# Kernel optimization log

Hardware: AMD Instinct MI355X
Metric: run time of the kernel (lower is better)

Reference implementation:

```python
import jax, jax.numpy as jnp
import numpy as np

D, H, DH, L, FF, P, IMG, NPR = 768, 12, 64, 12, 3072, 16, 224, 8
SCALE = 0.125  # 1/sqrt(64), hardcoded in source
DEEP_G = 12


def layernorm(x, g, b, eps=1e-5):
    mu = jnp.mean(x, axis=-1, keepdims=True)
    var = jnp.var(x, axis=-1, keepdims=True)
    return (x - mu) * jax.lax.rsqrt(var + eps) * g + b


def quick_gelu(x):  # CLIP's QuickGELU
    return x * jax.nn.sigmoid(1.702 * x)


def setup_inputs() -> dict:
    key = jax.random.key(0)
    ks = jax.random.split(key, 32)
    rn = lambda k, shape, s=0.02: (jax.random.normal(k, shape, jnp.float32) * s)
    B = 64
    return {
        "image": jax.random.normal(ks[0], (B, 3, IMG, IMG), jnp.float32),
        "g_prompt": rn(ks[1], (B, L, NPR, D)),
        "patch_w": rn(ks[2], (D, 3, P, P)),            # OIHW conv kernel (no bias in CLIP)
        "cls_emb": rn(ks[3], (D,)),
        "pos_emb": rn(ks[4], (1 + (IMG // P) ** 2, D)),  # [197, 768]
        "pre_g": jnp.ones((D,)), "pre_b": jnp.zeros((D,)),
        "ln1_g": jnp.ones((L, D)), "ln1_b": jnp.zeros((L, D)),
        "qw": rn(ks[5], (L, D, D)), "qb": jnp.zeros((L, D)),
        "kw": rn(ks[6], (L, D, D)), "kb": jnp.zeros((L, D)),
        "vw": rn(ks[7], (L, D, D)), "vb": jnp.zeros((L, D)),
        "ow": rn(ks[8], (L, D, D)), "ob": jnp.zeros((L, D)),
        "ln2_g": jnp.ones((L, D)), "ln2_b": jnp.zeros((L, D)),
        "fc1_w": rn(ks[9], (L, FF, D)), "fc1_b": jnp.zeros((L, FF)),
        "fc2_w": rn(ks[10], (L, D, FF)), "fc2_b": jnp.zeros((L, D)),
        "post_g": jnp.ones((D,)), "post_b": jnp.zeros((D,)),
    }


def reference(image, g_prompt, patch_w, cls_emb, pos_emb, pre_g, pre_b,
              ln1_g, ln1_b, qw, qb, kw, kb, vw, vb, ow, ob,
              ln2_g, ln2_b, fc1_w, fc1_b, fc2_w, fc2_b, post_g, post_b):
    B = image.shape[0]
    # --- embeddings: patch conv (stride=patch, VALID), flatten, prepend CLS, add pos ---
    feat = jax.lax.conv_general_dilated(
        image, patch_w, window_strides=(P, P), padding="VALID",
        dimension_numbers=("NCHW", "OIHW", "NCHW"))          # [B, D, 14, 14]
    feat = feat.reshape(B, D, -1).transpose(0, 2, 1)           # [B, 196, D]
    cls = jnp.broadcast_to(cls_emb, (B, 1, D))
    x = jnp.concatenate([cls, feat], axis=1) + pos_emb[None]   # [B, 197, D]
    # --- append prompts for layer 0, pre-layernorm ---
    x = jnp.concatenate([x, g_prompt[:, 0]], axis=1)           # [B, 205, D]
    x = layernorm(x, pre_g, pre_b)
    S = x.shape[1]
    for i in range(L):
        if i > 0 and i < DEEP_G:  # replace method: swap in fresh prompts
            x = jnp.concatenate([x[:, :-NPR], g_prompt[:, i]], axis=1)
        # --- attention ---
        res = x
        h = layernorm(x, ln1_g[i], ln1_b[i])
        q = (jnp.einsum("bsd,od->bso", h, qw[i]) + qb[i]) * SCALE
        k = jnp.einsum("bsd,od->bso", h, kw[i]) + kb[i]
        v = jnp.einsum("bsd,od->bso", h, vw[i]) + vb[i]
        q = q.reshape(B, S, H, DH)
        k = k.reshape(B, S, H, DH)
        v = v.reshape(B, S, H, DH)
        w = jnp.einsum("bihd,bjhd->bhij", q, k)
        w = jax.nn.softmax(w, axis=-1)
        a = jnp.einsum("bhij,bjhd->bihd", w, v).reshape(B, S, D)
        x = res + (jnp.einsum("bsd,od->bso", a, ow[i]) + ob[i])
        # --- MLP (QuickGELU) ---
        res = x
        h = layernorm(x, ln2_g[i], ln2_b[i])
        h = quick_gelu(jnp.einsum("bsd,fd->bsf", h, fc1_w[i]) + fc1_b[i])
        x = res + (jnp.einsum("bsf,df->bsd", h, fc2_w[i]) + fc2_b[i])
    return layernorm(x[:, 0, :], post_g, post_b)               # [B, D]
```

## Files before the change

kernel.cpp:

```cpp
#include <hip/hip_runtime.h>
#include <hip/hip_bf16.h>

typedef __hip_bfloat16 bf16;
typedef __attribute__((ext_vector_type(8))) __bf16 bf16x8;
typedef __attribute__((ext_vector_type(4))) float f32x4;

static constexpr int B_   = 64;
static constexpr int S_   = 205;
static constexpr int D_   = 768;
static constexpr int FF_  = 3072;
static constexpr int L_   = 12;
static constexpr int MTOK = B_ * S_;
static constexpr int MPAD = 13184;
static constexpr int MP_  = 12544;

static constexpr size_t OFF_QKVW = 0;
static constexpr size_t OFF_OW   = OFF_QKVW + (size_t)12*2304*768*2;
static constexpr size_t OFF_FC1W = OFF_OW   + (size_t)12*768*768*2;
static constexpr size_t OFF_FC2W = OFF_FC1W + (size_t)12*3072*768*2;
static constexpr size_t OFF_PW   = OFF_FC2W + (size_t)12*768*3072*2;
static constexpr size_t OFF_QKVB = OFF_PW   + (size_t)768*768*2;
static constexpr size_t OFF_X    = OFF_QKVB + (size_t)12*2304*4;
static constexpr size_t OFF_H    = OFF_X    + (size_t)MPAD*768*4;
static constexpr size_t OFF_QKV  = OFF_H    + (size_t)MPAD*768*2;
static constexpr size_t OFF_FF   = OFF_QKV  + (size_t)MPAD*2304*2;

__device__ __forceinline__ f32x4 mfma16(bf16x8 a, bf16x8 b, f32x4 c) {
  return __builtin_amdgcn_mfma_f32_16x16x32_bf16(a, b, c, 0, 0, 0);
}

__device__ __forceinline__ void async_ld16(const bf16* g, bf16* l) {
  __builtin_amdgcn_global_load_lds(
      (const __attribute__((address_space(1))) unsigned int*)g,
      (__attribute__((address_space(3))) unsigned int*)l, 16, 0, 0);
}

__global__ __launch_bounds__(256) void cvt_bf16_kernel(const float* __restrict__ src,
                                                       bf16* __restrict__ dst, int n4) {
  int i = blockIdx.x * 256 + threadIdx.x;
  if (i >= n4) return;
  float4 v = ((const float4*)src)[i];
  int e = i * 4;
  dst[e + 0] = __float2bfloat16(v.x);
  dst[e + 1] = __float2bfloat16(v.y);
  dst[e + 2] = __float2bfloat16(v.z);
  dst[e + 3] = __float2bfloat16(v.w);
}

__global__ __launch_bounds__(256) void cvt_qkvw_kernel(const float* __restrict__ qw,
    const float* __restrict__ kw, const float* __restrict__ vw, bf16* __restrict__ dst) {
  int i = blockIdx.x * 256 + threadIdx.x;
  const int total = 12 * 2304 * 768 / 4;
  if (i >= total) return;
  int e = i * 4;
  int l = e / (2304 * 768);
  int r = e - l * (2304 * 768);
  int o = r / 768;
  int d = r - o * 768;
  const float* src;
  if (o < 768)       src = qw + ((size_t)l * 768 + o) * 768 + d;
  else if (o < 1536) src = kw + ((size_t)l * 768 + (o - 768)) * 768 + d;
  else               src = vw + ((size_t)l * 768 + (o - 1536)) * 768 + d;
  float4 v = *(const float4*)src;
  dst[e + 0] = __float2bfloat16(v.x);
  dst[e + 1] = __float2bfloat16(v.y);
  dst[e + 2] = __float2bfloat16(v.z);
  dst[e + 3] = __float2bfloat16(v.w);
}

__global__ __launch_bounds__(256) void cvt_qkvb_kernel(const float* __restrict__ qb,
    const float* __restrict__ kb, const float* __restrict__ vb, float* __restrict__ dst) {
  int i = blockIdx.x * 256 + threadIdx.x;
  if (i >= 12 * 2304) return;
  int l = i / 2304, o = i - l * 2304;
  float v = (o < 768) ? qb[l * 768 + o] : (o < 1536) ? kb[l * 768 + o - 768] : vb[l * 768 + o - 1536];
  dst[i] = v;
}

__global__ __launch_bounds__(256) void im2col_kernel(const float* __restrict__ img,
                                                     bf16* __restrict__ dst) {
  int idx = blockIdx.x * 256 + threadIdx.x;
  if (idx >= MP_ * 768) return;
  int k = idx % 768;
  int m = idx / 768;
  int b = m / 196, p = m - b * 196;
  int py = p / 14, px = p - py * 14;
  int c = k >> 8, rr = k & 255, kh = rr >> 4, kw_ = rr & 15;
  dst[idx] = __float2bfloat16(img[((size_t)(b * 3 + c) * 224 + py * 16 + kh) * 224 + px * 16 + kw_]);
}

__global__ __launch_bounds__(256) void assemble_kernel(const float* __restrict__ feat,
    const float* __restrict__ cls, const float* __restrict__ pos,
    const float* __restrict__ gp, float* __restrict__ x) {
  int idx = blockIdx.x * 256 + threadIdx.x;
  if (idx >= MTOK * 768) return;
  int d = idx % 768;
  int t = idx / 768;
  int s = t % 205;
  int b = t / 205;
  float v;
  if (s == 0)        v = cls[d] + pos[d];
  else if (s < 197)  v = feat[((size_t)b * 196 + (s - 1)) * 768 + d] + pos[(size_t)s * 768 + d];
  else               v = gp[(((size_t)b * 12 + 0) * 8 + (s - 197)) * 768 + d];
  x[idx] = v;
}

__global__ __launch_bounds__(256) void prompt_replace_kernel(const float* __restrict__ gp,
                                                             float* __restrict__ x, int layer) {
  int idx = blockIdx.x * 256 + threadIdx.x;
  if (idx >= B_ * 8 * 768) return;
  int d = idx % 768;
  int t = idx / 768;
  int j = t & 7, b = t >> 3;
  x[((size_t)(b * 205 + 197 + j)) * 768 + d] = gp[(((size_t)b * 12 + layer) * 8 + j) * 768 + d];
}

__global__ __launch_bounds__(256) void ln_kernel(const float* __restrict__ x, int irs,
    const float* __restrict__ g, const float* __restrict__ be,
    void* __restrict__ out, int ors, int out_bf16, int nrows) {
  int row = blockIdx.x * 4 + (threadIdx.x >> 6);
  if (row >= nrows) return;
  int lane = threadIdx.x & 63;
  const float* xr = x + (size_t)row * irs;
  float v[12];
  float s = 0.f;
#pragma unroll
  for (int i = 0; i < 12; ++i) { v[i] = xr[lane + 64 * i]; s += v[i]; }
#pragma unroll
  for (int m = 1; m < 64; m <<= 1) s += __shfl_xor(s, m, 64);
  float mu = s * (1.f / 768.f);
  float ss = 0.f;
#pragma unroll
  for (int i = 0; i < 12; ++i) { float dd = v[i] - mu; ss += dd * dd; }
#pragma unroll
  for (int m = 1; m < 64; m <<= 1) ss += __shfl_xor(ss, m, 64);
  float rstd = rsqrtf(ss * (1.f / 768.f) + 1e-5f);
#pragma unroll
  for (int i = 0; i < 12; ++i) {
    int d = lane + 64 * i;
    float o = (v[i] - mu) * rstd * g[d] + be[d];
    if (out_bf16) ((bf16*)out)[(size_t)row * ors + d] = __float2bfloat16(o);
    else          ((float*)out)[(size_t)row * ors + d] = o;
  }
}

__global__ __launch_bounds__(256) void gemm_kernel(
    const bf16* __restrict__ A, int lda,
    const bf16* __restrict__ W, int ldw,
    const float* __restrict__ bias,
    void* __restrict__ out, int ldo, int out_bf16,
    const float* __restrict__ residual, int ldr,
    int act, float scale, int scale_limit,
    int M_valid, int K) {
  __shared__ __align__(16) bf16 As[128 * 32];
  __shared__ __align__(16) bf16 Bs[128 * 32];
  const int tid = threadIdx.x;
  const int wave = tid >> 6, lane = tid & 63;
  const int quad = lane >> 4, l16 = lane & 15;
  const int m0 = blockIdx.x * 128, n0 = blockIdx.y * 128;
  const int wm = (wave & 1) * 64, wn = (wave >> 1) * 64;

  const bf16* a_src = A + (size_t)(m0 + (tid >> 2)) * lda + (tid & 3) * 8;
  const bf16* b_src = W + (size_t)(n0 + (tid >> 2)) * ldw + (tid & 3) * 8;
  bf16* As_w0 = As + (wave * 16) * 32;
  bf16* As_w1 = As + (64 + wave * 16) * 32;
  bf16* Bs_w0 = Bs + (wave * 16) * 32;
  bf16* Bs_w1 = Bs + (64 + wave * 16) * 32;
  const size_t a_step = (size_t)64 * lda;
  const size_t b_step = (size_t)64 * ldw;

  f32x4 acc[4][4];
#pragma unroll
  for (int tm = 0; tm < 4; ++tm)
#pragma unroll
    for (int tn = 0; tn < 4; ++tn) {
      f32x4 z = {0.f, 0.f, 0.f, 0.f};
      acc[tm][tn] = z;
    }

  for (int k0 = 0; k0 < K; k0 += 32) {
    async_ld16(a_src + k0, As_w0);
    async_ld16(a_src + a_step + k0, As_w1);
    async_ld16(b_src + k0, Bs_w0);
    async_ld16(b_src + b_step + k0, Bs_w1);
    __syncthreads();
    bf16x8 af[4], bfr[4];
#pragma unroll
    for (int tm = 0; tm < 4; ++tm)
      af[tm] = *(const bf16x8*)(As + (wm + tm * 16 + l16) * 32 + quad * 8);
#pragma unroll
    for (int tn = 0; tn < 4; ++tn)
      bfr[tn] = *(const bf16x8*)(Bs + (wn + tn * 16 + l16) * 32 + quad * 8);
#pragma unroll
    for (int tm = 0; tm < 4; ++tm)
#pragma unroll
      for (int tn = 0; tn < 4; ++tn)
        acc[tm][tn] = mfma16(af[tm], bfr[tn], acc[tm][tn]);
    __syncthreads();
  }

#pragma unroll
  for (int tm = 0; tm < 4; ++tm) {
#pragma unroll
    for (int tn = 0; tn < 4; ++tn) {
      const int col = n0 + wn + tn * 16 + l16;
      const float bv = bias ? bias[col] : 0.f;
      const float sc = (col < scale_limit) ? scale : 1.f;
#pragma unroll
      for (int r = 0; r < 4; ++r) {
        const int row = m0 + wm + tm * 16 + quad * 4 + r;
        if (row < M_valid) {
          float v = (acc[tm][tn][r] + bv) * sc;
          if (residual) v += residual[(size_t)row * ldr + col];
          if (act) v = v / (1.f + __expf(-1.702f * v));
          if (out_bf16) ((bf16*)out)[(size_t)row * ldo + col] = __float2bfloat16(v);
          else          ((float*)out)[(size_t)row * ldo + col] = v;
        }
      }
    }
  }
}

__global__ __launch_bounds__(256) void attn_kernel(const bf16* __restrict__ qkv,
                                                   bf16* __restrict__ outb) {
  __shared__ __align__(16) bf16 Ks[208 * 72];
  __shared__ __align__(16) bf16 Vt[64 * 232];
  __shared__ __align__(16) bf16 Pc[4 * 16 * 40];
  const int h = blockIdx.x, b = blockIdx.y;
  const int tid = threadIdx.x;
  const int wave = tid >> 6, lane = tid & 63, quad = lane >> 4, l16 = lane & 15;
  const size_t rowbase = (size_t)b * 205;

  for (int idx = tid; idx < 208 * 8; idx += 256) {
    int s = idx >> 3, c = idx & 7;
    uint4 val = {0u, 0u, 0u, 0u};
    if (s < 205) val = *(const uint4*)(qkv + (rowbase + s) * 2304 + 768 + h * 64 + c * 8);
    *(uint4*)(Ks + s * 72 + c * 8) = val;
  }
  for (int idx = tid; idx < 224 * 8; idx += 256) {
    int s = idx >> 3, c = idx & 7;
    bf16 tmp[8];
    if (s < 205) {
      *(uint4*)tmp = *(const uint4*)(qkv + (rowbase + s) * 2304 + 1536 + h * 64 + c * 8);
    } else {
#pragma unroll
      for (int j = 0; j < 8; ++j) tmp[j] = __float2bfloat16(0.f);
    }
#pragma unroll
    for (int j = 0; j < 8; ++j) Vt[(c * 8 + j) * 232 + s] = tmp[j];
  }
  __syncthreads();

  bf16* Pm = Pc + wave * (16 * 40);

  for (int t = 0; t < 4; ++t) {
    const int it = t * 4 + wave;
    if (it >= 13) continue;
    const int row0 = it * 16;
    const bf16* qr = qkv + (rowbase + row0 + l16) * 2304 + h * 64;
    bf16x8 qf0 = *(const bf16x8*)(qr + quad * 8);
    bf16x8 qf1 = *(const bf16x8*)(qr + 32 + quad * 8);

    f32x4 sc[13];
#pragma unroll
    for (int nt = 0; nt < 13; ++nt) {
      f32x4 a = {0.f, 0.f, 0.f, 0.f};
      const bf16* kr = Ks + (nt * 16 + l16) * 72 + quad * 8;
      a = mfma16(qf0, *(const bf16x8*)kr, a);
      a = mfma16(qf1, *(const bf16x8*)(kr + 32), a);
      sc[nt] = a;
    }
    if (l16 >= 13) {
#pragma unroll
      for (int r = 0; r < 4; ++r) sc[12][r] = -1e30f;
    }

    float inv[4];
#pragma unroll
    for (int r = 0; r < 4; ++r) {
      float m = sc[0][r];
#pragma unroll
      for (int nt = 1; nt < 13; ++nt) m = fmaxf(m, sc[nt][r]);
      m = fmaxf(m, __shfl_xor(m, 1, 64));
      m = fmaxf(m, __shfl_xor(m, 2, 64));
      m = fmaxf(m, __shfl_xor(m, 4, 64));
      m = fmaxf(m, __shfl_xor(m, 8, 64));
      float su = 0.f;
#pragma unroll
      for (int nt = 0; nt < 13; ++nt) { float e = __expf(sc[nt][r] - m); sc[nt][r] = e; su += e; }
      su += __shfl_xor(su, 1, 64);
      su += __shfl_xor(su, 2, 64);
      su += __shfl_xor(su, 4, 64);
      su += __shfl_xor(su, 8, 64);
      inv[r] = 1.f / su;
    }

    f32x4 o0 = {0.f,0.f,0.f,0.f}, o1 = {0.f,0.f,0.f,0.f}, o2 = {0.f,0.f,0.f,0.f}, o3 = {0.f,0.f,0.f,0.f};
#pragma unroll
    for (int ks = 0; ks < 7; ++ks) {
#pragma unroll
      for (int half = 0; half < 2; ++half) {
        const int nt = ks * 2 + half;
#pragma unroll
        for (int r = 0; r < 4; ++r) {
          float pv = (nt < 13) ? sc[nt][r] * inv[r] : 0.f;
          Pm[(quad * 4 + r) * 40 + half * 16 + l16] = __float2bfloat16(pv);
        }
      }
      asm volatile("s_waitcnt lgkmcnt(0)" ::: "memory");
      bf16x8 pf = *(const bf16x8*)(Pm + l16 * 40 + quad * 8);
      const bf16* vb_ = Vt + l16 * 232 + ks * 32 + quad * 8;
      o0 = mfma16(pf, *(const bf16x8*)(vb_ + 0 * 16 * 232), o0);
      o1 = mfma16(pf, *(const bf16x8*)(vb_ + 1 * 16 * 232), o1);
      o2 = mfma16(pf, *(const bf16x8*)(vb_ + 2 * 16 * 232), o2);
      o3 = mfma16(pf, *(const bf16x8*)(vb_ + 3 * 16 * 232), o3);
      asm volatile("s_waitcnt lgkmcnt(0)" ::: "memory");
    }
#pragma unroll
    for (int r = 0; r < 4; ++r) {
      const int s = row0 + quad * 4 + r;
      if (s < 205) {
        bf16* op = outb + (rowbase + s) * 768 + h * 64 + l16;
        op[0]  = __float2bfloat16(o0[r]);
        op[16] = __float2bfloat16(o1[r]);
        op[32] = __float2bfloat16(o2[r]);
        op[48] = __float2bfloat16(o3[r]);
      }
    }
  }
}

extern "C" void kernel_launch(void* const* d_in, const int* in_sizes, int n_in,
                              void* d_out, int out_size, void* d_ws, size_t ws_size,
                              hipStream_t stream) {
  const float* image  = (const float*)d_in[0];
  const float* gp     = (const float*)d_in[1];
  const float* patchw = (const float*)d_in[2];
  const float* clse   = (const float*)d_in[3];
  const float* pose   = (const float*)d_in[4];
  const float* pre_g  = (const float*)d_in[5];
  const float* pre_b  = (const float*)d_in[6];
  const float* ln1_g  = (const float*)d_in[7];
  const float* ln1_b  = (const float*)d_in[8];
  const float* qw     = (const float*)d_in[9];
  const float* qb     = (const float*)d_in[10];
  const float* kw     = (const float*)d_in[11];
  const float* kb     = (const float*)d_in[12];
  const float* vw     = (const float*)d_in[13];
  const float* vb     = (const float*)d_in[14];
  const float* ow     = (const float*)d_in[15];
  const float* ob     = (const float*)d_in[16];
  const float* ln2_g  = (const float*)d_in[17];
  const float* ln2_b  = (const float*)d_in[18];
  const float* fc1w   = (const float*)d_in[19];
  const float* fc1b   = (const float*)d_in[20];
  const float* fc2w   = (const float*)d_in[21];
  const float* fc2b   = (const float*)d_in[22];
  const float* postg  = (const float*)d_in[23];
  const float* postb  = (const float*)d_in[24];

  char* ws = (char*)d_ws;
  bf16*  qkvw   = (bf16*)(ws + OFF_QKVW);
  bf16*  oww    = (bf16*)(ws + OFF_OW);
  bf16*  fc1wb  = (bf16*)(ws + OFF_FC1W);
  bf16*  fc2wb  = (bf16*)(ws + OFF_FC2W);
  bf16*  pwb    = (bf16*)(ws + OFF_PW);
  float* qkvbias= (float*)(ws + OFF_QKVB);
  float* x      = (float*)(ws + OFF_X);
  bf16*  h      = (bf16*)(ws + OFF_H);
  bf16*  qkvbuf = (bf16*)(ws + OFF_QKV);
  bf16*  ffbuf  = (bf16*)(ws + OFF_FF);
  float* feat   = (float*)(ws + OFF_FF);

  cvt_qkvw_kernel<<<20736, 256, 0, stream>>>(qw, kw, vw, qkvw);
  cvt_bf16_kernel<<<6912, 256, 0, stream>>>(ow, oww, 12 * 768 * 768 / 4);
  cvt_bf16_kernel<<<27648, 256, 0, stream>>>(fc1w, fc1wb, 12 * 3072 * 768 / 4);
  cvt_bf16_kernel<<<27648, 256, 0, stream>>>(fc2w, fc2wb, 12 * 768 * 3072 / 4);
  cvt_bf16_kernel<<<576, 256, 0, stream>>>(patchw, pwb, 768 * 768 / 4);
  cvt_qkvb_kernel<<<108, 256, 0, stream>>>(qb, kb, vb, qkvbias);

  im2col_kernel<<<37632, 256, 0, stream>>>(image, h);
  gemm_kernel<<<dim3(98, 6), 256, 0, stream>>>(h, 768, pwb, 768, nullptr,
      feat, 768, 0, nullptr, 0, 0, 1.f, 0, MP_, 768);
  assemble_kernel<<<39360, 256, 0, stream>>>(feat, clse, pose, gp, x);
  ln_kernel<<<3280, 256, 0, stream>>>(x, 768, pre_g, pre_b, x, 768, 0, MTOK);

  for (int i = 0; i < L_; ++i) {
    if (i > 0)
      prompt_replace_kernel<<<1536, 256, 0, stream>>>(gp, x, i);
    ln_kernel<<<3280, 256, 0, stream>>>(x, 768, ln1_g + i * 768, ln1_b + i * 768, h, 768, 1, MTOK);
    gemm_kernel<<<dim3(103, 18), 256, 0, stream>>>(h, 768,
        qkvw + (size_t)i * 2304 * 768, 768, qkvbias + i * 2304,
        qkvbuf, 2304, 1, nullptr, 0, 0, 0.125f, 768, MTOK, 768);
    attn_kernel<<<dim3(12, 64), 256, 0, stream>>>(qkvbuf, h);
    gemm_kernel<<<dim3(103, 6), 256, 0, stream>>>(h, 768,
        oww + (size_t)i * 768 * 768, 768, ob + i * 768,
        x, 768, 0, x, 768, 0, 1.f, 0, MTOK, 768);
    ln_kernel<<<3280, 256, 0, stream>>>(x, 768, ln2_g + i * 768, ln2_b + i * 768, h, 768, 1, MTOK);
    gemm_kernel<<<dim3(103, 24), 256, 0, stream>>>(h, 768,
        fc1wb + (size_t)i * 3072 * 768, 768, fc1b + i * 3072,
        ffbuf, 3072, 1, nullptr, 0, 1, 1.f, 0, MTOK, 768);
    gemm_kernel<<<dim3(103, 6), 256, 0, stream>>>(ffbuf, 3072,
        fc2wb + (size_t)i * 768 * 3072, 3072, fc2b + i * 768,
        x, 768, 0, x, 768, 0, 1.f, 0, MTOK, 3072);
  }

  ln_kernel<<<16, 256, 0, stream>>>(x, 205 * 768, postg, postb, (float*)d_out, 768, 0, 64);
}
```

Before: 7.205 ms.

## Widen GEMM K-tile to 64, XOR-swizzle LDS, add grouped block rasterization

The GEMM now stages a 128x64 K-slice per iteration instead of 128x32, which halves the number of barriers per output tile. It XOR-swizzles the LDS column layout so fragment reads avoid bank conflicts. Blocks are launched on a 1D grid and remapped into groups of 8 M-tiles so neighbouring blocks share A and W tiles in L2. LDS use doubles to 32KB per block, which may reduce occupancy, and there is still no double buffering.

```diff
diff --git a/kernel.cpp b/kernel.cpp
--- a/kernel.cpp
+++ b/kernel.cpp
@@ -144,6 +144,8 @@
   }
 }
 
+static constexpr int SG = 8;
+
 __global__ __launch_bounds__(256) void gemm_kernel(
     const bf16* __restrict__ A, int lda,
     const bf16* __restrict__ W, int ldw,
@@ -151,23 +153,39 @@
     void* __restrict__ out, int ldo, int out_bf16,
     const float* __restrict__ residual, int ldr,
     int act, float scale, int scale_limit,
-    int M_valid, int K) {
-  __shared__ __align__(16) bf16 As[128 * 32];
-  __shared__ __align__(16) bf16 Bs[128 * 32];
+    int M_valid, int K, int gm, int gn) {
+  __shared__ __align__(16) bf16 As[128 * 64];
+  __shared__ __align__(16) bf16 Bs[128 * 64];
   const int tid = threadIdx.x;
   const int wave = tid >> 6, lane = tid & 63;
   const int quad = lane >> 4, l16 = lane & 15;
-  const int m0 = blockIdx.x * 128, n0 = blockIdx.y * 128;
+
+  const int bid = blockIdx.x;
+  const int super = bid / (SG * gn);
+  const int m_base = super * SG;
+  const int Gc = min(SG, gm - m_base);
+  const int rem = bid - super * (SG * gn);
+  const int n_blk = rem / Gc;
+  const int m_blk = m_base + (rem - n_blk * Gc);
+  const int m0 = m_blk * 128, n0 = n_blk * 128;
+
   const int wm = (wave & 1) * 64, wn = (wave >> 1) * 64;
 
-  const bf16* a_src = A + (size_t)(m0 + (tid >> 2)) * lda + (tid & 3) * 8;
-  const bf16* b_src = W + (size_t)(n0 + (tid >> 2)) * ldw + (tid & 3) * 8;
-  bf16* As_w0 = As + (wave * 16) * 32;
-  bf16* As_w1 = As + (64 + wave * 16) * 32;
-  bf16* Bs_w0 = Bs + (wave * 16) * 32;
-  bf16* Bs_w1 = Bs + (64 + wave * 16) * 32;
-  const size_t a_step = (size_t)64 * lda;
-  const size_t b_step = (size_t)64 * ldw;
+  const int lrow = lane >> 3;
+  const int lcol = ((lane & 7) ^ lrow) * 8;
+  const bf16* a_stage = A + (size_t)(m0 + wave * 32 + lrow) * lda + lcol;
+  const bf16* b_stage = W + (size_t)(n0 + wave * 32 + lrow) * ldw + lcol;
+  bf16* as_dst0 = As + (wave * 32 + 0) * 64;
+  bf16* as_dst1 = As + (wave * 32 + 8) * 64;
+  bf16* as_dst2 = As + (wave * 32 + 16) * 64;
+  bf16* as_dst3 = As + (wave * 32 + 24) * 64;
+  bf16* bs_dst0 = Bs + (wave * 32 + 0) * 64;
+  bf16* bs_dst1 = Bs + (wave * 32 + 8) * 64;
+  bf16* bs_dst2 = Bs + (wave * 32 + 16) * 64;
+  bf16* bs_dst3 = Bs + (wave * 32 + 24) * 64;
+  const size_t a8 = (size_t)8 * lda, b8 = (size_t)8 * ldw;
+
+  const int sw = l16 & 7;
 
   f32x4 acc[4][4];
 #pragma unroll
@@ -178,24 +196,47 @@
       acc[tm][tn] = z;
     }
 
-  for (int k0 = 0; k0 < K; k0 += 32) {
-    async_ld16(a_src + k0, As_w0);
-    async_ld16(a_src + a_step + k0, As_w1);
-    async_ld16(b_src + k0, Bs_w0);
-    async_ld16(b_src + b_step + k0, Bs_w1);
+  for (int k0 = 0; k0 < K; k0 += 64) {
+    async_ld16(a_stage + k0,          as_dst0);
+    async_ld16(a_stage + a8 + k0,     as_dst1);
+    async_ld16(a_stage + 2*a8 + k0,   as_dst2);
+    async_ld16(a_stage + 3*a8 + k0,   as_dst3);
+    async_ld16(b_stage + k0,          bs_dst0);
+    async_ld16(b_stage + b8 + k0,     bs_dst1);
+    async_ld16(b_stage + 2*b8 + k0,   bs_dst2);
+    async_ld16(b_stage + 3*b8 + k0,   bs_dst3);
     __syncthreads();
-    bf16x8 af[4], bfr[4];
-#pragma unroll
-    for (int tm = 0; tm < 4; ++tm)
-      af[tm] = *(const bf16x8*)(As + (wm + tm * 16 + l16) * 32 + quad * 8);
-#pragma unroll
-    for (int tn = 0; tn < 4; ++tn)
-      bfr[tn] = *(const bf16x8*)(Bs + (wn + tn * 16 + l16) * 32 + quad * 8);
-#pragma unroll
-    for (int tm = 0; tm < 4; ++tm)
+
+    {
+      bf16x8 af[4], bfr[4];
+      const int c0 = ((quad ^ sw) * 8);
+#pragma unroll
+      for (int tm = 0; tm < 4; ++tm)
+        af[tm] = *(const bf16x8*)(As + (wm + tm * 16 + l16) * 64 + c0);
 #pragma unroll
       for (int tn = 0; tn < 4; ++tn)
-        acc[tm][tn] = mfma16(af[tm], bfr[tn], acc[tm][tn]);
+        bfr[tn] = *(const bf16x8*)(Bs + (wn + tn * 16 + l16) * 64 + c0);
+#pragma unroll
+      for (int tm = 0; tm < 4; ++tm)
+#pragma unroll
+        for (int tn = 0; tn < 4; ++tn)
+          acc[tm][tn] = mfma16(af[tm], bfr[tn], acc[tm][tn]);
+    }
+    {
+      bf16x8 af[4], bfr[4];
+      const int c1 = (((quad + 4) ^ sw) * 8);
+#pragma unroll
+      for (int tm = 0; tm < 4; ++tm)
+        af[tm] = *(const bf16x8*)(As + (wm + tm * 16 + l16) * 64 + c1);
+#pragma unroll
+      for (int tn = 0; tn < 4; ++tn)
+        bfr[tn] = *(const bf16x8*)(Bs + (wn + tn * 16 + l16) * 64 + c1);
+#pragma unroll
+      for (int tm = 0; tm < 4; ++tm)
+#pragma unroll
+        for (int tn = 0; tn < 4; ++tn)
+          acc[tm][tn] = mfma16(af[tm], bfr[tn], acc[tm][tn]);
+    }
     __syncthreads();
   }
 
@@ -380,8 +421,8 @@
   cvt_qkvb_kernel<<<108, 256, 0, stream>>>(qb, kb, vb, qkvbias);
 
   im2col_kernel<<<37632, 256, 0, stream>>>(image, h);
-  gemm_kernel<<<dim3(98, 6), 256, 0, stream>>>(h, 768, pwb, 768, nullptr,
-      feat, 768, 0, nullptr, 0, 0, 1.f, 0, MP_, 768);
+  gemm_kernel<<<98 * 6, 256, 0, stream>>>(h, 768, pwb, 768, nullptr,
+      feat, 768, 0, nullptr, 0, 0, 1.f, 0, MP_, 768, 98, 6);
   assemble_kernel<<<39360, 256, 0, stream>>>(feat, clse, pose, gp, x);
   ln_kernel<<<3280, 256, 0, stream>>>(x, 768, pre_g, pre_b, x, 768, 0, MTOK);
 
@@ -389,20 +430,20 @@
     if (i > 0)
       prompt_replace_kernel<<<1536, 256, 0, stream>>>(gp, x, i);
     ln_kernel<<<3280, 256, 0, stream>>>(x, 768, ln1_g + i * 768, ln1_b + i * 768, h, 768, 1, MTOK);
-    gemm_kernel<<<dim3(103, 18), 256, 0, stream>>>(h, 768,
+    gemm_kernel<<<103 * 18, 256, 0, stream>>>(h, 768,
         qkvw + (size_t)i * 2304 * 768, 768, qkvbias + i * 2304,
-        qkvbuf, 2304, 1, nullptr, 0, 0, 0.125f, 768, MTOK, 768);
+        qkvbuf, 2304, 1, nullptr, 0, 0, 0.125f, 768, MTOK, 768, 103, 18);
     attn_kernel<<<dim3(12, 64), 256, 0, stream>>>(qkvbuf, h);
-    gemm_kernel<<<dim3(103, 6), 256, 0, stream>>>(h, 768,
+    gemm_kernel<<<103 * 6, 256, 0, stream>>>(h, 768,
         oww + (size_t)i * 768 * 768, 768, ob + i * 768,
-        x, 768, 0, x, 768, 0, 1.f, 0, MTOK, 768);
+        x, 768, 0, x, 768, 0, 1.f, 0, MTOK, 768, 103, 6);
     ln_kernel<<<3280, 256, 0, stream>>>(x, 768, ln2_g + i * 768, ln2_b + i * 768, h, 768, 1, MTOK);
-    gemm_kernel<<<dim3(103, 24), 256, 0, stream>>>(h, 768,
+    gemm_kernel<<<103 * 24, 256, 0, stream>>>(h, 768,
         fc1wb + (size_t)i * 3072 * 768, 768, fc1b + i * 3072,
-        ffbuf, 3072, 1, nullptr, 0, 1, 1.f, 0, MTOK, 768);
-    gemm_kernel<<<dim3(103, 6), 256, 0, stream>>>(ffbuf, 3072,
+        ffbuf, 3072, 1, nullptr, 0, 1, 1.f, 0, MTOK, 768, 103, 24);
+    gemm_kernel<<<103 * 6, 256, 0, stream>>>(ffbuf, 3072,
         fc2wb + (size_t)i * 768 * 3072, 3072, fc2b + i * 768,
-        x, 768, 0, x, 768, 0, 1.f, 0, MTOK, 3072);
+        x, 768, 0, x, 768, 0, 1.f, 0, MTOK, 3072, 103, 6);
   }
 
   ln_kernel<<<16, 256, 0, stream>>>(x, 205 * 768, postg, postb, (float*)d_out, 768, 0, 64);
```

New measurement: 5.825 ms. -19.2%, faster.

## Replace LDS-staged GEMM with single-wave register-direct GEMM and grouped tile order

Applied to the files above, without the earlier changes.

The 4-wave GEMM that staged A and B tiles through shared memory with async loads and barriers is replaced by a one-wave-per-block kernel. Each wave loads 128x128 tile fragments straight from global memory into registers, double-buffered across K steps, so there is no LDS and no __syncthreads. Blocks are also remapped into supergroups of 8 M-tiles to improve L2 reuse of weight tiles. In exchange each wave now holds 256 accumulator registers plus two buffers of operand fragments, which is very heavy register pressure. There is also no data sharing between waves, so global and L2 traffic per FLOP rises, and occupancy drops to a single wave per block.

```diff
diff --git a/kernel.cpp b/kernel.cpp
--- a/kernel.cpp
+++ b/kernel.cpp
@@ -27,12 +27,6 @@
 
 __device__ __forceinline__ f32x4 mfma16(bf16x8 a, bf16x8 b, f32x4 c) {
   return __builtin_amdgcn_mfma_f32_16x16x32_bf16(a, b, c, 0, 0, 0);
-}
-
-__device__ __forceinline__ void async_ld16(const bf16* g, bf16* l) {
-  __builtin_amdgcn_global_load_lds(
-      (const __attribute__((address_space(1))) unsigned int*)g,
-      (__attribute__((address_space(3))) unsigned int*)l, 16, 0, 0);
 }
 
 __global__ __launch_bounds__(256) void cvt_bf16_kernel(const float* __restrict__ src,
@@ -144,73 +138,88 @@
   }
 }
 
-__global__ __launch_bounds__(256) void gemm_kernel(
+static constexpr int SG = 8;
+
+template<int TM, int TN>
+__global__ __launch_bounds__(64, 1) void gemm1w_kernel(
     const bf16* __restrict__ A, int lda,
     const bf16* __restrict__ W, int ldw,
     const float* __restrict__ bias,
     void* __restrict__ out, int ldo, int out_bf16,
     const float* __restrict__ residual, int ldr,
     int act, float scale, int scale_limit,
-    int M_valid, int K) {
-  __shared__ __align__(16) bf16 As[128 * 32];
-  __shared__ __align__(16) bf16 Bs[128 * 32];
-  const int tid = threadIdx.x;
-  const int wave = tid >> 6, lane = tid & 63;
+    int M_valid, int K, int gm, int gn) {
+  constexpr int FM = TM / 16, FN = TN / 16;
+  const int lane = threadIdx.x;
   const int quad = lane >> 4, l16 = lane & 15;
-  const int m0 = blockIdx.x * 128, n0 = blockIdx.y * 128;
-  const int wm = (wave & 1) * 64, wn = (wave >> 1) * 64;
-
-  const bf16* a_src = A + (size_t)(m0 + (tid >> 2)) * lda + (tid & 3) * 8;
-  const bf16* b_src = W + (size_t)(n0 + (tid >> 2)) * ldw + (tid & 3) * 8;
-  bf16* As_w0 = As + (wave * 16) * 32;
-  bf16* As_w1 = As + (64 + wave * 16) * 32;
-  bf16* Bs_w0 = Bs + (wave * 16) * 32;
-  bf16* Bs_w1 = Bs + (64 + wave * 16) * 32;
-  const size_t a_step = (size_t)64 * lda;
-  const size_t b_step = (size_t)64 * ldw;
-
-  f32x4 acc[4][4];
-#pragma unroll
-  for (int tm = 0; tm < 4; ++tm)
-#pragma unroll
-    for (int tn = 0; tn < 4; ++tn) {
+
+  const int bid = blockIdx.x;
+  const int super = bid / (SG * gn);
+  const int m_base = super * SG;
+  const int Gc = min(SG, gm - m_base);
+  const int rem = bid - super * (SG * gn);
+  const int n_blk = rem / Gc;
+  const int m_blk = m_base + (rem - n_blk * Gc);
+  const int m0 = m_blk * TM, n0 = n_blk * TN;
+
+  const bf16* a_base = A + (size_t)(m0 + l16) * lda + quad * 8;
+  const bf16* b_base = W + (size_t)(n0 + l16) * ldw + quad * 8;
+
+  f32x4 acc[FM][FN];
+#pragma unroll
+  for (int fm = 0; fm < FM; ++fm)
+#pragma unroll
+    for (int fn = 0; fn < FN; ++fn) {
       f32x4 z = {0.f, 0.f, 0.f, 0.f};
-      acc[tm][tn] = z;
-    }
-
-  for (int k0 = 0; k0 < K; k0 += 32) {
-    async_ld16(a_src + k0, As_w0);
-    async_ld16(a_src + a_step + k0, As_w1);
-    async_ld16(b_src + k0, Bs_w0);
-    async_ld16(b_src + b_step + k0, Bs_w1);
-    __syncthreads();
-    bf16x8 af[4], bfr[4];
-#pragma unroll
-    for (int tm = 0; tm < 4; ++tm)
-      af[tm] = *(const bf16x8*)(As + (wm + tm * 16 + l16) * 32 + quad * 8);
-#pragma unroll
-    for (int tn = 0; tn < 4; ++tn)
-      bfr[tn] = *(const bf16x8*)(Bs + (wn + tn * 16 + l16) * 32 + quad * 8);
-#pragma unroll
-    for (int tm = 0; tm < 4; ++tm)
-#pragma unroll
-      for (int tn = 0; tn < 4; ++tn)
-        acc[tm][tn] = mfma16(af[tm], bfr[tn], acc[tm][tn]);
-    __syncthreads();
-  }
-
-#pragma unroll
-  for (int tm = 0; tm < 4; ++tm) {
-#pragma unroll
-    for (int tn = 0; tn < 4; ++tn) {
-      const int col = n0 + wn + tn * 16 + l16;
-      const float bv = bias ? bias[col] : 0.f;
-      const float sc = (col < scale_limit) ? scale : 1.f;
+      acc[fm][fn] = z;
+    }
+
+  bf16x8 a0[FM], b0[FN], a1[FM], b1[FN];
+
+#define LOAD_AB(av, bv, kk)                                                    \
+  {                                                                            \
+    _Pragma("unroll")                                                          \
+    for (int i = 0; i < FM; ++i)                                               \
+      av[i] = *(const bf16x8*)(a_base + (size_t)i * 16 * lda + (kk));          \
+    _Pragma("unroll")                                                          \
+    for (int j = 0; j < FN; ++j)                                               \
+      bv[j] = *(const bf16x8*)(b_base + (size_t)j * 16 * ldw + (kk));          \
+  }
+
+#define MFMA_AB(av, bv)                                                        \
+  {                                                                            \
+    _Pragma("unroll")                                                          \
+    for (int fm = 0; fm < FM; ++fm)                                            \
+      _Pragma("unroll")                                                        \
+      for (int fn = 0; fn < FN; ++fn)                                          \
+        acc[fm][fn] = mfma16(av[fm], bv[fn], acc[fm][fn]);                     \
+  }
+
+  LOAD_AB(a0, b0, 0);
+  for (int k0 = 32; k0 < K - 32; k0 += 64) {
+    LOAD_AB(a1, b1, k0);
+    MFMA_AB(a0, b0);
+    LOAD_AB(a0, b0, k0 + 32);
+    MFMA_AB(a1, b1);
+  }
+  LOAD_AB(a1, b1, K - 32);
+  MFMA_AB(a0, b0);
+  MFMA_AB(a1, b1);
+#undef LOAD_AB
+#undef MFMA_AB
+
+#pragma unroll
+  for (int fn = 0; fn < FN; ++fn) {
+    const int col = n0 + fn * 16 + l16;
+    const float bv = bias ? bias[col] : 0.f;
+    const float sc = (col < scale_limit) ? scale : 1.f;
+#pragma unroll
+    for (int fm = 0; fm < FM; ++fm) {
 #pragma unroll
       for (int r = 0; r < 4; ++r) {
-        const int row = m0 + wm + tm * 16 + quad * 4 + r;
+        const int row = m0 + fm * 16 + quad * 4 + r;
         if (row < M_valid) {
-          float v = (acc[tm][tn][r] + bv) * sc;
+          float v = (acc[fm][fn][r] + bv) * sc;
           if (residual) v += residual[(size_t)row * ldr + col];
           if (act) v = v / (1.f + __expf(-1.702f * v));
           if (out_bf16) ((bf16*)out)[(size_t)row * ldo + col] = __float2bfloat16(v);
@@ -380,8 +389,8 @@
   cvt_qkvb_kernel<<<108, 256, 0, stream>>>(qb, kb, vb, qkvbias);
 
   im2col_kernel<<<37632, 256, 0, stream>>>(image, h);
-  gemm_kernel<<<dim3(98, 6), 256, 0, stream>>>(h, 768, pwb, 768, nullptr,
-      feat, 768, 0, nullptr, 0, 0, 1.f, 0, MP_, 768);
+  gemm1w_kernel<128, 128><<<98 * 6, 64, 0, stream>>>(h, 768, pwb, 768, nullptr,
+      feat, 768, 0, nullptr, 0, 0, 1.f, 0, MP_, 768, 98, 6);
   assemble_kernel<<<39360, 256, 0, stream>>>(feat, clse, pose, gp, x);
   ln_kernel<<<3280, 256, 0, stream>>>(x, 768, pre_g, pre_b, x, 768, 0, MTOK);
 
@@ -389,20 +398,20 @@
     if (i > 0)
       prompt_replace_kernel<<<1536, 256, 0, stream>>>(gp, x, i);
     ln_kernel<<<3280, 256, 0, stream>>>(x, 768, ln1_g + i * 768, ln1_b + i * 768, h, 768, 1, MTOK);
-    gemm_kernel<<<dim3(103, 18), 256, 0, stream>>>(h, 768,
+    gemm1w_kernel<128, 128><<<103 * 18, 64, 0, stream>>>(h, 768,
         qkvw + (size_t)i * 2304 * 768, 768, qkvbias + i * 2304,
-        qkvbuf, 2304, 1, nullptr, 0, 0, 0.125f, 768, MTOK, 768);
+        qkvbuf, 2304, 1, nullptr, 0, 0, 0.125f, 768, MTOK, 768, 103, 18);
     attn_kernel<<<dim3(12, 64), 256, 0, stream>>>(qkvbuf, h);
-    gemm_kernel<<<dim3(103, 6), 256, 0, stream>>>(h, 768,
+    gemm1w_kernel<128, 128><<<103 * 6, 64, 0, stream>>>(h, 768,
         oww + (size_t)i * 768 * 768, 768, ob + i * 768,
-        x, 768, 0, x, 768, 0, 1.f, 0, MTOK, 768);
+        x, 768, 0, x, 768, 0, 1.f, 0, MTOK, 768, 103, 6);
     ln_kernel<<<3280, 256, 0, stream>>>(x, 768, ln2_g + i * 768, ln2_b + i * 768, h, 768, 1, MTOK);
-    gemm_kernel<<<dim3(103, 24), 256, 0, stream>>>(h, 768,
+    gemm1w_kernel<128, 128><<<103 * 24, 64, 0, stream>>>(h, 768,
         fc1wb + (size_t)i * 3072 * 768, 768, fc1b + i * 3072,
-        ffbuf, 3072, 1, nullptr, 0, 1, 1.f, 0, MTOK, 768);
-    gemm_kernel<<<dim3(103, 6), 256, 0, stream>>>(ffbuf, 3072,
+        ffbuf, 3072, 1, nullptr, 0, 1, 1.f, 0, MTOK, 768, 103, 24);
+    gemm1w_kernel<128, 128><<<103 * 6, 64, 0, stream>>>(ffbuf, 3072,
         fc2wb + (size_t)i * 768 * 3072, 3072, fc2b + i * 768,
-        x, 768, 0, x, 768, 0, 1.f, 0, MTOK, 3072);
+        x, 768, 0, x, 768, 0, 1.f, 0, MTOK, 3072, 103, 6);
   }
 
   ln_kernel<<<16, 256, 0, stream>>>(x, 205 * 768, postg, postb, (float*)d_out, 768, 0, 64);
```

After: 12.56 ms. 1.74x slower.
